# Performance work log

Hardware: AMD Instinct MI355X
Metric: run time of the kernel (lower is better)

## Reference

```python
import jax, jax.numpy as jnp
import numpy as np

C = 10  # cluster gap window; repo-level global constant in the original code


def _per_neuron(v, label):
    """Faithful vectorized translation of the per-(batch,neuron) Python loops.

    v:     [T] membrane potential trace
    label: scalar int target cluster count
    Returns (loss_contribution, num_cluster).
    """
    T = v.shape[0]
    t = jnp.arange(T, dtype=jnp.int32)
    spk = v >= 0.0                                   # spike positions (v >= 0)
    # exclusive prefix counts of spikes: csp[i] = #spikes in v[:i]
    csp = jnp.concatenate([jnp.zeros(1, jnp.int32), jnp.cumsum(spk.astype(jnp.int32))])
    lo = jnp.clip(t - C, 0, T)
    # a spike starts a new cluster iff no spike in the preceding C steps
    cnt_prev = csp[t] - csp[lo]
    is_start = spk & (cnt_prev == 0)
    num_cluster = jnp.sum(is_start.astype(jnp.int32))
    vmax = jnp.max(v)

    # ---- excess branch (label > num_cluster) ----
    # mask[t] = 1 iff some spike lies in [t-C, t+C]  (union of [first-C, last+C] per cluster)
    hi = jnp.clip(t + C + 1, 0, T)
    mask = (csp[hi] - csp[lo]) > 0
    full0 = jnp.all(mask)
    NEG = jnp.asarray(-1e30, v.dtype)
    m0 = jnp.max(jnp.where(mask, NEG, v))            # max over unmasked times (iter 0)
    tm = jnp.argmax(v)                               # original uses global argmax of v
    win = (t >= tm - C // 2) & (t <= tm + C // 2)
    mask2 = mask | win                               # mask after first loop iteration (fixed thereafter)
    full2 = jnp.all(mask2)
    # if mask2 full, remaining iterations pick a spike value (random in original; spikes have v>=0,
    # we use the deterministic surrogate vmax which is always a spike value when spikes exist)
    m_rest = jnp.where(full2, vmax, jnp.max(jnp.where(mask2, NEG, v)))
    label_f = label.astype(v.dtype)
    ncf = num_cluster.astype(v.dtype)
    dE = jnp.maximum(label_f - ncf, 1.0)             # safe denominator (branch-gated below)
    mean_excess = (m0 + (dE - 1.0) * m_rest) / dE
    excess_loss = jnp.where(full0, vmax, -mean_excess)

    # ---- deficit branch (label < num_cluster) ----
    BIG = T + 2 * C + 2
    lt = jax.lax.cummax(jnp.where(spk, t, -BIG))                 # nearest spike <= t
    rt = jax.lax.cummin(jnp.where(spk, t, BIG)[::-1])[::-1]      # nearest spike >= t
    in_span = (rt - lt) <= C                                     # t inside [first,last] of a cluster
    cid = jnp.cumsum(is_start.astype(jnp.int32)) - 1             # cluster id at time t
    K = T // (C + 1) + 1                                         # max possible clusters
    seg = jnp.where(in_span, cid, K)
    rec = jax.ops.segment_max(v, seg, num_segments=K + 1)[:K]    # per-cluster span max
    POS = jnp.asarray(1e30, v.dtype)
    rec = jnp.where(jnp.arange(K) < num_cluster, rec, POS)
    rec = jnp.sort(rec)                                          # ascending, real clusters first
    dD = jnp.maximum(ncf - label_f, 1.0)
    deficit_loss = jnp.sum(jnp.where(jnp.arange(K) < (num_cluster - label), rec, 0.0)) / dD

    contrib = jnp.where(label > num_cluster, excess_loss,
                        jnp.where(label < num_cluster, deficit_loss, 0.0))
    return contrib, num_cluster


def setup_inputs() -> dict:
    key = jax.random.key(0)
    k1, k2, k3 = jax.random.split(key, 3)
    B, T, N = 256, 500, 128
    vmem = jax.random.normal(k1, (B, T, N), dtype=jnp.float32)
    vlastmem = jax.random.normal(k2, (B, T, N), dtype=jnp.float32)
    labels_t = jax.random.randint(k3, (B, N), 0, 5, dtype=jnp.int32)
    return {"vmem": vmem, "vlastmem": vlastmem, "labels_t": labels_t, "ratio": 1}


def reference(vmem, vlastmem, labels_t, ratio):
    # vlastmem and ratio are unused in the original forward; kept for signature fidelity.
    vv = jnp.transpose(vmem, (0, 2, 1))  # [B, N, T]
    contrib, nclus = jax.vmap(jax.vmap(_per_neuron))(vv, labels_t)
    loss = jnp.sum(contrib)
    spike_output = nclus.astype(jnp.float32)  # [B, N] cluster counts
    return loss, spike_output
```

## Files before the change

### kernel.cpp

```cpp
#include <hip/hip_runtime.h>

namespace {
constexpr int CC    = 10;
constexpr int TT    = 500;
constexpr int NN    = 128;
constexpr int G     = 10;
constexpr int LSEG  = TT / G;
constexpr int HALO  = CC;
constexpr int LROWS = 72;
constexpr int NF4   = (LROWS * NN / 4) / NN;
constexpr int NSLOT = 10;
constexpr int MAXG  = TT / (CC + 1) + 1;
}

__global__ __launch_bounds__(128, 2)
void seg_scan_kernel(const float* __restrict__ vmem, float* __restrict__ ws) {
    const int s   = blockIdx.x;
    const int b   = blockIdx.y;
    const int tid = threadIdx.x;
    const int a   = s * LSEG;
    int ldstart = a - HALO;
    ldstart = ldstart < 0 ? 0 : ldstart;
    ldstart = ldstart > TT - LROWS ? TT - LROWS : ldstart;
    const int shift = a - ldstart;

    __shared__ __align__(16) float buf[LROWS * NN];
    __shared__ float stg[5 * NN];

    const float4* __restrict__ g4 =
        (const float4*)(vmem + ((size_t)b * TT + ldstart) * NN);
    float4 r[NF4];
    #pragma unroll
    for (int i = 0; i < NF4; ++i) r[i] = g4[tid + NN * i];
    #pragma unroll
    for (int i = 0; i < 5; ++i) stg[i * NN + tid] = 0.0f;
    float4* l4 = (float4*)buf;
    #pragma unroll
    for (int i = 0; i < NF4; ++i) l4[tid + NN * i] = r[i];
    __syncthreads();

    int   ls = -(1 << 20), lcount = 0, hdne = 0, tmn = 0, hasu = 0;
    float ccm = -1e30f, rmax = -1e30f, hdm = -1e30f, vmx = -1e30f, m0 = -1e30f;
    const bool firstSeg = (s == 0), lastSeg = (s == G - 1);

    #pragma unroll
    for (int ofs = -HALO; ofs < LSEG + HALO; ++ofs) {
        const int t = a + ofs;
        const bool invalid = (firstSeg && ofs < 0) || (lastSeg && ofs >= LSEG);
        const float v = invalid ? -1.0f : buf[(ofs + shift) * NN + tid];
        const bool spike = v >= 0.0f;
        if (ofs >= 0 && ofs < LSEG) {
            const float rm2 = fmaxf(rmax, v);
            if (spike) {
                if (t - ls > CC) {
                    if (lcount > 0) stg[(lcount - 1) * NN + tid] = ccm;
                    ccm = v; ++lcount;
                } else if (lcount == 0) { hdne = 1; hdm = fmaxf(hdm, rm2); }
                else ccm = fmaxf(ccm, rm2);
                rmax = -1e30f;
            } else rmax = rm2;
            if (v > vmx) { vmx = v; tmn = t; }
        }
        if (spike) ls = t;
        if (ofs >= HALO) {
            const float vu = buf[(ofs - HALO + shift) * NN + tid];
            if (ls < t - 2 * CC) { hasu = 1; if (vu > m0) m0 = vu; }
        }
    }
    if (lcount > 0) stg[(lcount - 1) * NN + tid] = ccm;

    float* __restrict__ wsl = ws + (size_t)(b * G + s) * NSLOT * NN + tid;
    #pragma unroll
    for (int i = 0; i < 5; ++i) wsl[i * NN] = stg[i * NN + tid];
    const int packed = lcount | (hdne << 3) | (hasu << 4) | (tmn << 5);
    wsl[5 * NN] = __int_as_float(packed);
    wsl[6 * NN] = hdm;
    wsl[7 * NN] = rmax;
    wsl[8 * NN] = vmx;
    wsl[9 * NN] = m0;
}

__global__ __launch_bounds__(128, 2)
void merge_kernel(const float* __restrict__ vmem, const float* __restrict__ ws,
                  const int* __restrict__ labels, float* __restrict__ out) {
    const int b = blockIdx.x, tid = threadIdx.x, lane = tid & 63;
    __shared__ float gl[MAXG * NN];
    __shared__ float wbuf[2][512];
    __shared__ float red[2];

    float cm[G][5], hd[G], tg[G], vx[G], mm[G]; int pk[G];
    const float* __restrict__ wsb = ws + (size_t)b * G * NSLOT * NN + tid;
    #pragma unroll
    for (int s2 = 0; s2 < G; ++s2) {
        const float* p = wsb + (size_t)s2 * NSLOT * NN;
        #pragma unroll
        for (int i = 0; i < 5; ++i) cm[s2][i] = p[i * NN];
        pk[s2] = __float_as_int(p[5 * NN]);
        hd[s2] = p[6 * NN];
        tg[s2] = p[7 * NN];
        vx[s2] = p[8 * NN];
        mm[s2] = p[9 * NN];
    }

    int g = 0, g_nc = 0, g_hasu = 0, g_tm = 0;
    bool open = false; float cur = -1e30f, ptg = -1e30f;
    float g_vmax = -1e30f, g_m0 = -1e30f;
    #pragma unroll
    for (int s2 = 0; s2 < G; ++s2) {
        const int k   = pk[s2] & 7;
        const int hne = (pk[s2] >> 3) & 1;
        g_nc += k; g_hasu |= (pk[s2] >> 4) & 1;
        if (vx[s2] > g_vmax) { g_vmax = vx[s2]; g_tm = pk[s2] >> 5; }
        if (mm[s2] > g_m0) g_m0 = mm[s2];
        if (open) {
            if (hne) { cur = fmaxf(cur, fmaxf(ptg, hd[s2])); ptg = tg[s2]; }
            if (k > 0 || !hne) { gl[g * NN + tid] = cur; ++g; open = false; }
        }
        if (k > 0) {
            #pragma unroll
            for (int i = 0; i < 4; ++i)
                if (i < k - 1) { gl[g * NN + tid] = cm[s2][i]; ++g; }
            float last = cm[s2][4];
            if (k == 1) last = cm[s2][0];
            else if (k == 2) last = cm[s2][1];
            else if (k == 3) last = cm[s2][2];
            else if (k == 4) last = cm[s2][3];
            cur = last; open = true; ptg = tg[s2];
        }
    }
    if (open) { gl[g * NN + tid] = cur; ++g; }

    const int label = labels[b * NN + tid];

    const bool need2 = (label > g_nc) && g_hasu && (label - g_nc >= 2);
    float mrest = g_vmax;
    unsigned long long bal = __ballot(need2);
    if (bal) {
        float* wb = wbuf[tid >> 6];
        const float* colbase = vmem + (size_t)b * TT * NN;
        while (bal) {
            const int f = __ffsll((unsigned long long)bal) - 1;
            bal &= bal - 1;
            const int   nf    = (tid & 64) | f;
            const int   tmf   = __shfl(g_tm, f);
            const float vmaxf = __shfl(g_vmax, f);
            #pragma unroll
            for (int j = 0; j < 8; ++j) {
                const int t = lane * 8 + j;
                wb[t] = (t < TT) ? colbase[(size_t)t * NN + nf] : -1.0f;
            }
            __threadfence_block();
            int ls2 = -1000, lh = 0; float lm = -1e30f;
            const int u0 = lane * 8;
            for (int t2 = u0 - 10; t2 < u0 + 18; ++t2) {
                const float v = (t2 >= 0 && t2 < 512) ? wb[t2] : -1.0f;
                if (v >= 0.0f) ls2 = t2;
                const int u = t2 - 10;
                if (u >= u0 && u < u0 + 8 && u < TT) {
                    if (ls2 < u - 10 && (u < tmf - CC / 2 || u > tmf + CC / 2)) {
                        lh = 1; const float vu = wb[u]; if (vu > lm) lm = vu;
                    }
                }
            }
            #pragma unroll
            for (int off = 32; off > 0; off >>= 1) {
                lm = fmaxf(lm, __shfl_down(lm, off));
                lh |= __shfl_down(lh, off);
            }
            const float res = __shfl(lh ? lm : vmaxf, 0);
            if (lane == f) mrest = res;
            __threadfence_block();
        }
    }

    float contrib = 0.0f;
    if (label > g_nc) {
        if (!g_hasu) contrib = g_vmax;
        else {
            const float dE = (float)(label - g_nc);
            contrib = -((g_m0 + (dE - 1.0f) * mrest) / dE);
        }
    } else if (label < g_nc) {
        const int kk = g_nc - label;
        float ssum = 0.0f;
        for (int i = 0; i < kk; ++i) {
            float mn = 1e30f; int mj = 0;
            for (int jj = 0; jj < g_nc; ++jj) {
                const float x = gl[jj * NN + tid];
                if (x < mn) { mn = x; mj = jj; }
            }
            ssum += mn; gl[mj * NN + tid] = 1e30f;
        }
        contrib = ssum / (float)kk;
    }

    out[1 + b * NN + tid] = (float)g_nc;

    float w = contrib;
    #pragma unroll
    for (int off = 32; off > 0; off >>= 1) w += __shfl_down(w, off);
    if (lane == 0) red[tid >> 6] = w;
    __syncthreads();
    if (tid == 0) atomicAdd(out, red[0] + red[1]);
}

extern "C" void kernel_launch(void* const* d_in, const int* in_sizes, int n_in,
                              void* d_out, int out_size, void* d_ws, size_t ws_size,
                              hipStream_t stream) {
    const float* vmem   = (const float*)d_in[0];
    const int*   labels = (const int*)d_in[2];
    float*       out    = (float*)d_out;
    float*       ws     = (float*)d_ws;

    const int B = in_sizes[2] / NN;

    hipMemsetAsync(out, 0, sizeof(float), stream);
    hipLaunchKernelGGL(seg_scan_kernel, dim3(G, B), dim3(NN), 0, stream, vmem, ws);
    hipLaunchKernelGGL(merge_kernel, dim3(B), dim3(NN), 0, stream, vmem, ws, labels, out);
}
```

Baseline: 172.5 us.

## Stream segment scan through register chunks and split merge into wave-sized blocks

```diff
diff --git a/kernel.cpp b/kernel.cpp
--- a/kernel.cpp
+++ b/kernel.cpp
@@ -7,66 +7,73 @@
 constexpr int G     = 10;
 constexpr int LSEG  = TT / G;
 constexpr int HALO  = CC;
-constexpr int LROWS = 72;
-constexpr int NF4   = (LROWS * NN / 4) / NN;
 constexpr int NSLOT = 10;
 constexpr int MAXG  = TT / (CC + 1) + 1;
 }
 
-__global__ __launch_bounds__(128, 2)
+__global__ __launch_bounds__(128, 5)
 void seg_scan_kernel(const float* __restrict__ vmem, float* __restrict__ ws) {
     const int s   = blockIdx.x;
     const int b   = blockIdx.y;
     const int tid = threadIdx.x;
     const int a   = s * LSEG;
-    int ldstart = a - HALO;
-    ldstart = ldstart < 0 ? 0 : ldstart;
-    ldstart = ldstart > TT - LROWS ? TT - LROWS : ldstart;
-    const int shift = a - ldstart;
-
-    __shared__ __align__(16) float buf[LROWS * NN];
+    const float* __restrict__ col = vmem + (size_t)b * TT * NN + tid;
+
     __shared__ float stg[5 * NN];
 
-    const float4* __restrict__ g4 =
-        (const float4*)(vmem + ((size_t)b * TT + ldstart) * NN);
-    float4 r[NF4];
-    #pragma unroll
-    for (int i = 0; i < NF4; ++i) r[i] = g4[tid + NN * i];
-    #pragma unroll
-    for (int i = 0; i < 5; ++i) stg[i * NN + tid] = 0.0f;
-    float4* l4 = (float4*)buf;
-    #pragma unroll
-    for (int i = 0; i < NF4; ++i) l4[tid + NN * i] = r[i];
-    __syncthreads();
+    float b0[10], b1[10], b2[10], b3[10] = {};
+    auto load = [&](float (&d)[10], int c) {
+        #pragma unroll
+        for (int j = 0; j < 10; ++j) {
+            int t = a + (-HALO + 10 * c + j);
+            t = t < 0 ? 0 : (t > TT - 1 ? TT - 1 : t);
+            d[j] = col[(size_t)t * NN];
+        }
+    };
 
     int   ls = -(1 << 20), lcount = 0, hdne = 0, tmn = 0, hasu = 0;
     float ccm = -1e30f, rmax = -1e30f, hdm = -1e30f, vmx = -1e30f, m0 = -1e30f;
     const bool firstSeg = (s == 0), lastSeg = (s == G - 1);
-
-    #pragma unroll
-    for (int ofs = -HALO; ofs < LSEG + HALO; ++ofs) {
-        const int t = a + ofs;
-        const bool invalid = (firstSeg && ofs < 0) || (lastSeg && ofs >= LSEG);
-        const float v = invalid ? -1.0f : buf[(ofs + shift) * NN + tid];
-        const bool spike = v >= 0.0f;
-        if (ofs >= 0 && ofs < LSEG) {
-            const float rm2 = fmaxf(rmax, v);
-            if (spike) {
-                if (t - ls > CC) {
-                    if (lcount > 0) stg[(lcount - 1) * NN + tid] = ccm;
-                    ccm = v; ++lcount;
-                } else if (lcount == 0) { hdne = 1; hdm = fmaxf(hdm, rm2); }
-                else ccm = fmaxf(ccm, rm2);
-                rmax = -1e30f;
-            } else rmax = rm2;
-            if (v > vmx) { vmx = v; tmn = t; }
-        }
-        if (spike) ls = t;
-        if (ofs >= HALO) {
-            const float vu = buf[(ofs - HALO + shift) * NN + tid];
-            if (ls < t - 2 * CC) { hasu = 1; if (vu > m0) m0 = vu; }
-        }
-    }
+    #pragma unroll
+    for (int i = 0; i < 5; ++i) stg[i * NN + tid] = 0.0f;
+
+    auto scan = [&](const float (&cur)[10], const float (&prev)[10], int c) {
+        #pragma unroll
+        for (int j = 0; j < 10; ++j) {
+            const int ofs = -HALO + 10 * c + j;
+            const int t   = a + ofs;
+            float v = cur[j];
+            if ((ofs < 0 && firstSeg) || (ofs >= LSEG && lastSeg)) v = -1.0f;
+            const bool spike = v >= 0.0f;
+            if (ofs >= 0 && ofs < LSEG) {
+                const float rm2 = fmaxf(rmax, v);
+                if (spike) {
+                    if (t - ls > CC) {
+                        if (lcount > 0) stg[(lcount - 1) * NN + tid] = ccm;
+                        ccm = v; ++lcount;
+                    } else if (lcount == 0) { hdne = 1; hdm = fmaxf(hdm, rm2); }
+                    else ccm = fmaxf(ccm, rm2);
+                    rmax = -1e30f;
+                } else rmax = rm2;
+                if (v > vmx) { vmx = v; tmn = t; }
+            }
+            if (spike) ls = t;
+            if (ofs >= HALO) {
+                const float vu = prev[j];
+                if (ls < t - 2 * CC) { hasu = 1; if (vu > m0) m0 = vu; }
+            }
+        }
+    };
+
+    load(b0, 0); load(b1, 1);
+    load(b2, 2); scan(b0, b3, 0);
+    load(b3, 3); scan(b1, b0, 1);
+    load(b0, 4); scan(b2, b1, 2);
+    load(b1, 5); scan(b3, b2, 3);
+    load(b2, 6); scan(b0, b3, 4);
+    scan(b1, b0, 5);
+    scan(b2, b1, 6);
+
     if (lcount > 0) stg[(lcount - 1) * NN + tid] = ccm;
 
     float* __restrict__ wsl = ws + (size_t)(b * G + s) * NSLOT * NN + tid;
@@ -80,97 +87,91 @@
     wsl[9 * NN] = m0;
 }
 
-__global__ __launch_bounds__(128, 2)
+__global__ __launch_bounds__(64)
 void merge_kernel(const float* __restrict__ vmem, const float* __restrict__ ws,
                   const int* __restrict__ labels, float* __restrict__ out) {
-    const int b = blockIdx.x, tid = threadIdx.x, lane = tid & 63;
-    __shared__ float gl[MAXG * NN];
-    __shared__ float wbuf[2][512];
-    __shared__ float red[2];
-
-    float cm[G][5], hd[G], tg[G], vx[G], mm[G]; int pk[G];
-    const float* __restrict__ wsb = ws + (size_t)b * G * NSLOT * NN + tid;
-    #pragma unroll
-    for (int s2 = 0; s2 < G; ++s2) {
+    const int bb = blockIdx.x, lane = threadIdx.x;
+    const int b = bb >> 1, n = ((bb & 1) << 6) | lane;
+    __shared__ float gl[MAXG * 64];
+    __shared__ float wb[512];
+
+    const float* __restrict__ wsb = ws + (size_t)b * G * NSLOT * NN + n;
+    float f[2][10];
+    auto loadSeg = [&](int slot, int s2) {
         const float* p = wsb + (size_t)s2 * NSLOT * NN;
         #pragma unroll
-        for (int i = 0; i < 5; ++i) cm[s2][i] = p[i * NN];
-        pk[s2] = __float_as_int(p[5 * NN]);
-        hd[s2] = p[6 * NN];
-        tg[s2] = p[7 * NN];
-        vx[s2] = p[8 * NN];
-        mm[s2] = p[9 * NN];
-    }
+        for (int i = 0; i < 10; ++i) f[slot][i] = p[i * NN];
+    };
+    loadSeg(0, 0);
 
     int g = 0, g_nc = 0, g_hasu = 0, g_tm = 0;
     bool open = false; float cur = -1e30f, ptg = -1e30f;
     float g_vmax = -1e30f, g_m0 = -1e30f;
     #pragma unroll
     for (int s2 = 0; s2 < G; ++s2) {
-        const int k   = pk[s2] & 7;
-        const int hne = (pk[s2] >> 3) & 1;
-        g_nc += k; g_hasu |= (pk[s2] >> 4) & 1;
-        if (vx[s2] > g_vmax) { g_vmax = vx[s2]; g_tm = pk[s2] >> 5; }
-        if (mm[s2] > g_m0) g_m0 = mm[s2];
+        if (s2 + 1 < G) loadSeg((s2 + 1) & 1, s2 + 1);
+        const float (&d)[10] = f[s2 & 1];
+        const int pk = __float_as_int(d[5]);
+        const int k = pk & 7, hne = (pk >> 3) & 1;
+        g_nc += k; g_hasu |= (pk >> 4) & 1;
+        if (d[8] > g_vmax) { g_vmax = d[8]; g_tm = pk >> 5; }
+        if (d[9] > g_m0) g_m0 = d[9];
         if (open) {
-            if (hne) { cur = fmaxf(cur, fmaxf(ptg, hd[s2])); ptg = tg[s2]; }
-            if (k > 0 || !hne) { gl[g * NN + tid] = cur; ++g; open = false; }
+            if (hne) { cur = fmaxf(cur, fmaxf(ptg, d[6])); ptg = d[7]; }
+            if (k > 0 || !hne) { gl[g * 64 + lane] = cur; ++g; open = false; }
         }
         if (k > 0) {
             #pragma unroll
             for (int i = 0; i < 4; ++i)
-                if (i < k - 1) { gl[g * NN + tid] = cm[s2][i]; ++g; }
-            float last = cm[s2][4];
-            if (k == 1) last = cm[s2][0];
-            else if (k == 2) last = cm[s2][1];
-            else if (k == 3) last = cm[s2][2];
-            else if (k == 4) last = cm[s2][3];
-            cur = last; open = true; ptg = tg[s2];
+                if (i < k - 1) { gl[g * 64 + lane] = d[i]; ++g; }
+            float last = d[4];
+            if (k == 1) last = d[0];
+            else if (k == 2) last = d[1];
+            else if (k == 3) last = d[2];
+            else if (k == 4) last = d[3];
+            cur = last; open = true; ptg = d[7];
         }
     }
-    if (open) { gl[g * NN + tid] = cur; ++g; }
-
-    const int label = labels[b * NN + tid];
+    if (open) { gl[g * 64 + lane] = cur; ++g; }
+
+    const int label = labels[b * NN + n];
 
     const bool need2 = (label > g_nc) && g_hasu && (label - g_nc >= 2);
     float mrest = g_vmax;
     unsigned long long bal = __ballot(need2);
-    if (bal) {
-        float* wb = wbuf[tid >> 6];
-        const float* colbase = vmem + (size_t)b * TT * NN;
-        while (bal) {
-            const int f = __ffsll((unsigned long long)bal) - 1;
-            bal &= bal - 1;
-            const int   nf    = (tid & 64) | f;
-            const int   tmf   = __shfl(g_tm, f);
-            const float vmaxf = __shfl(g_vmax, f);
-            #pragma unroll
-            for (int j = 0; j < 8; ++j) {
-                const int t = lane * 8 + j;
-                wb[t] = (t < TT) ? colbase[(size_t)t * NN + nf] : -1.0f;
-            }
-            __threadfence_block();
-            int ls2 = -1000, lh = 0; float lm = -1e30f;
-            const int u0 = lane * 8;
-            for (int t2 = u0 - 10; t2 < u0 + 18; ++t2) {
-                const float v = (t2 >= 0 && t2 < 512) ? wb[t2] : -1.0f;
-                if (v >= 0.0f) ls2 = t2;
-                const int u = t2 - 10;
-                if (u >= u0 && u < u0 + 8 && u < TT) {
-                    if (ls2 < u - 10 && (u < tmf - CC / 2 || u > tmf + CC / 2)) {
-                        lh = 1; const float vu = wb[u]; if (vu > lm) lm = vu;
-                    }
+    const float* colbase = vmem + (size_t)b * TT * NN;
+    while (bal) {
+        const int fl = __ffsll((unsigned long long)bal) - 1;
+        bal &= bal - 1;
+        const int   nf    = ((bb & 1) << 6) | fl;
+        const int   tmf   = __shfl(g_tm, fl);
+        const float vmaxf = __shfl(g_vmax, fl);
+        #pragma unroll
+        for (int j = 0; j < 8; ++j) {
+            const int t = lane * 8 + j;
+            wb[t] = (t < TT) ? colbase[(size_t)t * NN + nf] : -1.0f;
+        }
+        __syncthreads();
+        int ls2 = -1000, lh = 0; float lm = -1e30f;
+        const int u0 = lane * 8;
+        for (int t2 = u0 - 10; t2 < u0 + 18; ++t2) {
+            const float v = (t2 >= 0 && t2 < 512) ? wb[t2] : -1.0f;
+            if (v >= 0.0f) ls2 = t2;
+            const int u = t2 - 10;
+            if (u >= u0 && u < u0 + 8 && u < TT) {
+                if (ls2 < u - 10 && (u < tmf - CC / 2 || u > tmf + CC / 2)) {
+                    lh = 1; const float vu = wb[u]; if (vu > lm) lm = vu;
                 }
             }
-            #pragma unroll
-            for (int off = 32; off > 0; off >>= 1) {
-                lm = fmaxf(lm, __shfl_down(lm, off));
-                lh |= __shfl_down(lh, off);
-            }
-            const float res = __shfl(lh ? lm : vmaxf, 0);
-            if (lane == f) mrest = res;
-            __threadfence_block();
-        }
+        }
+        #pragma unroll
+        for (int off = 32; off > 0; off >>= 1) {
+            lm = fmaxf(lm, __shfl_down(lm, off));
+            lh |= __shfl_down(lh, off);
+        }
+        const float res = __shfl(lh ? lm : vmaxf, 0);
+        if (lane == fl) mrest = res;
+        __syncthreads();
     }
 
     float contrib = 0.0f;
@@ -186,22 +187,20 @@
         for (int i = 0; i < kk; ++i) {
             float mn = 1e30f; int mj = 0;
             for (int jj = 0; jj < g_nc; ++jj) {
-                const float x = gl[jj * NN + tid];
+                const float x = gl[jj * 64 + lane];
                 if (x < mn) { mn = x; mj = jj; }
             }
-            ssum += mn; gl[mj * NN + tid] = 1e30f;
+            ssum += mn; gl[mj * 64 + lane] = 1e30f;
         }
         contrib = ssum / (float)kk;
     }
 
-    out[1 + b * NN + tid] = (float)g_nc;
+    out[1 + b * NN + n] = (float)g_nc;
 
     float w = contrib;
     #pragma unroll
     for (int off = 32; off > 0; off >>= 1) w += __shfl_down(w, off);
-    if (lane == 0) red[tid >> 6] = w;
-    __syncthreads();
-    if (tid == 0) atomicAdd(out, red[0] + red[1]);
+    if (lane == 0) atomicAdd(out, w);
 }
 
 extern "C" void kernel_launch(void* const* d_in, const int* in_sizes, int n_in,
@@ -216,5 +215,5 @@
 
     hipMemsetAsync(out, 0, sizeof(float), stream);
     hipLaunchKernelGGL(seg_scan_kernel, dim3(G, B), dim3(NN), 0, stream, vmem, ws);
-    hipLaunchKernelGGL(merge_kernel, dim3(B), dim3(NN), 0, stream, vmem, ws, labels, out);
-}
+    hipLaunchKernelGGL(merge_kernel, dim3(2 * B), dim3(64), 0, stream, vmem, ws, labels, out);
+}
```

Result: faster. 164.5 us (-4.6%).
